# Optimization experiments

Hardware: AMD Instinct MI355X
Metric: run time of the kernel (lower is better)

The kernel has to match this reference:

```python
import jax, jax.numpy as jnp
import numpy as np

B, T, D, H, L, DFF, MAXLEN = 4, 2048, 512, 8, 6, 2048, 2048
DK = D // H
SCALE = float(1.0 / np.sqrt(DK * 2))  # 1/sqrt(d_k*2)


def layer_norm(x, g, b, eps=1e-5):
    m = jnp.mean(x, axis=-1, keepdims=True)
    v = jnp.var(x, axis=-1, keepdims=True)
    return (x - m) / jnp.sqrt(v + eps) * g + b


def setup_inputs() -> dict:
    key = jax.random.key(0)
    it = iter(jax.random.split(key, 48))
    def n(shape, std=0.02):
        return jax.random.normal(next(it), shape, dtype=jnp.float32) * std
    inp = {}
    inp['x'] = jax.random.normal(next(it), (B, T), dtype=jnp.float32)
    inp['ip_w'] = n((1, D)); inp['ip_b'] = jnp.zeros((D,))
    inp['ip_ln_g'] = jnp.ones((D,)); inp['ip_ln_b'] = jnp.zeros((D,))
    inp['pos_embed'] = n((MAXLEN, D), 0.01)
    inp['pad_token'] = n((D,), 0.01)
    inp['Wq'] = n((L, D, D)); inp['bq'] = jnp.zeros((L, D))
    inp['Wk'] = n((L, D, D)); inp['bk'] = jnp.zeros((L, D))
    inp['Wv'] = n((L, D, D)); inp['bv'] = jnp.zeros((L, D))
    inp['Wo'] = n((L, D, D)); inp['bo'] = jnp.zeros((L, D))
    inp['ln1_g'] = jnp.ones((L, D)); inp['ln1_b'] = jnp.zeros((L, D))
    inp['ln2_g'] = jnp.ones((L, D)); inp['ln2_b'] = jnp.zeros((L, D))
    inp['W1'] = n((L, D, DFF)); inp['b1'] = jnp.zeros((L, DFF))
    inp['W2'] = n((L, DFF, D)); inp['b2'] = jnp.zeros((L, D))
    inp['gate1'] = jnp.full((L,), 0.1); inp['gate2'] = jnp.full((L,), 0.1)
    inp['fn_g'] = jnp.ones((D,)); inp['fn_b'] = jnp.zeros((D,))
    for p in ['bh', 'ah', 'ch']:
        inp[p + '_ln_g'] = jnp.ones((D,)); inp[p + '_ln_b'] = jnp.zeros((D,))
    inp['bh_w'] = n((D, 2), 0.01); inp['bh_b'] = jnp.zeros((2,))
    inp['ah_w'] = n((D, 1), 0.01); inp['ah_b'] = jnp.zeros((1,))
    inp['ch_w'] = n((D, 1), 0.01); inp['ch_b'] = jnp.zeros((1,))
    return inp


def _forward(x, ip_w, ip_b, ip_ln_g, ip_ln_b, pos_embed, pad_token,
             Wq, bq, Wk, bk, Wv, bv, Wo, bo,
             ln1_g, ln1_b, ln2_g, ln2_b, W1, b1, W2, b2, gate1, gate2,
             fn_g, fn_b, bh_ln_g, bh_ln_b, bh_w, bh_b,
             ah_ln_g, ah_ln_b, ah_w, ah_b, ch_ln_g, ch_ln_b, ch_w, ch_b):
    Bx, Tx = x.shape
    xc = jnp.clip(x, -10.0, 10.0)
    pad_mask = xc == -1.0  # [B,T]
    h = layer_norm(xc[..., None] @ ip_w + ip_b, ip_ln_g, ip_ln_b)  # [B,T,D]
    h = h + 0.1 * pos_embed[None, :Tx, :]
    h = jnp.where(pad_mask[..., None], pad_token, h)
    cmask = jnp.triu(jnp.full((Tx, Tx), -10000.0, dtype=h.dtype), k=1)  # additive causal mask
    for i in range(L):
        xn = layer_norm(h, ln1_g[i], ln1_b[i])
        def heads(w, b, xn=xn):
            return (xn @ w + b).reshape(Bx, Tx, H, DK).transpose(0, 2, 1, 3)
        q = heads(Wq[i], bq[i]); k = heads(Wk[i], bk[i]); v = heads(Wv[i], bv[i])
        q = q / jnp.maximum(jnp.linalg.norm(q, axis=-1, keepdims=True), 1e-8)
        k = k / jnp.maximum(jnp.linalg.norm(k, axis=-1, keepdims=True), 1e-8)
        scores = jnp.clip(jnp.einsum('bhtd,bhsd->bhts', q, k) * SCALE, -5.0, 5.0) + cmask
        a = jax.nn.softmax(scores / 1.5, axis=-1)
        o = jnp.einsum('bhts,bhsd->bhtd', a, v).transpose(0, 2, 1, 3).reshape(Bx, Tx, D)
        h = h + gate1[i] * ((o @ Wo[i] + bo[i]) * 0.5)
        xn2 = layer_norm(h, ln2_g[i], ln2_b[i])
        ffn = jax.nn.gelu(xn2 @ W1[i] + b1[i], approximate=False) @ W2[i] + b2[i]
        h = jnp.clip(h + gate2[i] * ffn, -10.0, 10.0)
    h = layer_norm(h, fn_g, fn_b)
    m = (~pad_mask).astype(h.dtype)[..., None]
    mean = (h * m).sum(axis=1) / jnp.maximum(m.sum(axis=1), 1.0)  # masked mean pool [B,D]
    binary = layer_norm(mean, bh_ln_g, bh_ln_b) @ bh_w + bh_b
    anomaly = layer_norm(mean, ah_ln_g, ah_ln_b) @ ah_w + ah_b
    caustic = jax.nn.sigmoid(layer_norm(mean, ch_ln_g, ch_ln_b) @ ch_w + ch_b)
    return jnp.concatenate([binary, anomaly, caustic], axis=-1)  # [B,4]


def reference(x, ip_w, ip_b, ip_ln_g, ip_ln_b, pos_embed, pad_token,
              Wq, bq, Wk, bk, Wv, bv, Wo, bo,
              ln1_g, ln1_b, ln2_g, ln2_b, W1, b1, W2, b2, gate1, gate2,
              fn_g, fn_b, bh_ln_g, bh_ln_b, bh_w, bh_b,
              ah_ln_g, ah_ln_b, ah_w, ah_b, ch_ln_g, ch_ln_b, ch_w, ch_b):
    return _forward(x, ip_w, ip_b, ip_ln_g, ip_ln_b, pos_embed, pad_token,
                    Wq, bq, Wk, bk, Wv, bv, Wo, bo,
                    ln1_g, ln1_b, ln2_g, ln2_b, W1, b1, W2, b2, gate1, gate2,
                    fn_g, fn_b, bh_ln_g, bh_ln_b, bh_w, bh_b,
                    ah_ln_g, ah_ln_b, ah_w, ah_b, ch_ln_g, ch_ln_b, ch_w, ch_b)
```

## Files before the change

### kernel.cpp

```cpp
#include <hip/hip_runtime.h>
#include <hip/hip_bf16.h>
#include <math.h>

constexpr int Bsz = 4, T = 2048, D = 512, H = 8, Lnum = 6, DFF = 2048, DK = 64;
constexpr int QS2 = 1024;
constexpr float K2 = 0.08838834764831845f / 1.5f;

typedef __attribute__((ext_vector_type(8))) short svec8;
typedef __attribute__((ext_vector_type(4))) float fvec4;

__device__ __forceinline__ fvec4 mfma16(svec8 a, svec8 b, fvec4 c) {
    return __builtin_amdgcn_mfma_f32_16x16x32_bf16(a, b, c, 0, 0, 0);
}
__device__ __forceinline__ unsigned short f2b(float f) {
    unsigned int u = __float_as_uint(f);
    u += 0x7fffu + ((u >> 16) & 1u);
    return (unsigned short)(u >> 16);
}
__device__ __forceinline__ unsigned int pk2b(float a, float b) {
    __hip_bfloat162 h = __float22bfloat162_rn(float2{a, b});
    return *(unsigned int*)&h;
}
__device__ __forceinline__ float wave_red_sum(float v) {
    for (int o = 32; o > 0; o >>= 1) v += __shfl_down(v, o, 64);
    return __shfl(v, 0, 64);
}
__device__ __forceinline__ void glds16(const unsigned short* g, unsigned short* l) {
    __builtin_amdgcn_global_load_lds(
        (const __attribute__((address_space(1))) unsigned int*)g,
        (__attribute__((address_space(3))) unsigned int*)l, 16, 0, 0);
}
#define FRAG(buf, row, kq) (*(const svec8*)((buf) + (((row) << 6) | ((((kq) ^ ((row) & 7))) << 3))))

__global__ __launch_bounds__(64)
void embed_kernel(const float* __restrict__ x, const float* __restrict__ ip_w,
                  const float* __restrict__ ip_b, const float* __restrict__ g,
                  const float* __restrict__ bta, const float* __restrict__ pos,
                  const float* __restrict__ pad_tok, float* __restrict__ h)
{
    int row = blockIdx.x;
    int t = row & (T - 1);
    int lane = threadIdx.x;
    float xv = x[row];
    float xc = fminf(fmaxf(xv, -10.f), 10.f);
    bool pad = (xc == -1.0f);
    float pre[8];
    float s = 0.f, s2 = 0.f;
#pragma unroll
    for (int j = 0; j < 8; j++) {
        int d = j * 64 + lane;
        float p = xc * ip_w[d] + ip_b[d];
        pre[j] = p; s += p; s2 += p * p;
    }
    s = wave_red_sum(s); s2 = wave_red_sum(s2);
    float m = s * (1.f / 512.f);
    float var = s2 * (1.f / 512.f) - m * m;
    float rstd = 1.f / sqrtf(var + 1e-5f);
#pragma unroll
    for (int j = 0; j < 8; j++) {
        int d = j * 64 + lane;
        float hv = (pre[j] - m) * rstd * g[d] + bta[d] + 0.1f * pos[(size_t)t * D + d];
        if (pad) hv = pad_tok[d];
        h[(size_t)row * D + d] = hv;
    }
}

__global__ __launch_bounds__(256)
void ln_kernel(const float* __restrict__ in, float* __restrict__ out,
               const float* __restrict__ g, const float* __restrict__ b)
{
    int row = blockIdx.x * 4 + (threadIdx.x >> 6);
    int lane = threadIdx.x & 63;
    const float* r = in + (size_t)row * D;
    float4 v0 = ((const float4*)r)[lane];
    float4 v1 = ((const float4*)r)[lane + 64];
    float s = v0.x + v0.y + v0.z + v0.w + v1.x + v1.y + v1.z + v1.w;
    float s2 = v0.x*v0.x + v0.y*v0.y + v0.z*v0.z + v0.w*v0.w
             + v1.x*v1.x + v1.y*v1.y + v1.z*v1.z + v1.w*v1.w;
    s = wave_red_sum(s); s2 = wave_red_sum(s2);
    float m = s * (1.f / 512.f);
    float var = s2 * (1.f / 512.f) - m * m;
    float rstd = 1.f / sqrtf(var + 1e-5f);
    float4 g0 = ((const float4*)g)[lane], g1 = ((const float4*)g)[lane + 64];
    float4 b0 = ((const float4*)b)[lane], b1 = ((const float4*)b)[lane + 64];
    float4 o0, o1;
    o0.x = (v0.x - m) * rstd * g0.x + b0.x; o0.y = (v0.y - m) * rstd * g0.y + b0.y;
    o0.z = (v0.z - m) * rstd * g0.z + b0.z; o0.w = (v0.w - m) * rstd * g0.w + b0.w;
    o1.x = (v1.x - m) * rstd * g1.x + b1.x; o1.y = (v1.y - m) * rstd * g1.y + b1.y;
    o1.z = (v1.z - m) * rstd * g1.z + b1.z; o1.w = (v1.w - m) * rstd * g1.w + b1.w;
    ((float4*)(out + (size_t)row * D))[lane] = o0;
    ((float4*)(out + (size_t)row * D))[lane + 64] = o1;
}

__global__ __launch_bounds__(256)
void ln_bf16_kernel(const float* __restrict__ in, unsigned short* __restrict__ out,
                    const float* __restrict__ g, const float* __restrict__ b)
{
    int row = blockIdx.x * 4 + (threadIdx.x >> 6);
    int lane = threadIdx.x & 63;
    const float* r = in + (size_t)row * D;
    float4 v0 = ((const float4*)r)[lane];
    float4 v1 = ((const float4*)r)[lane + 64];
    float s = v0.x + v0.y + v0.z + v0.w + v1.x + v1.y + v1.z + v1.w;
    float s2 = v0.x*v0.x + v0.y*v0.y + v0.z*v0.z + v0.w*v0.w
             + v1.x*v1.x + v1.y*v1.y + v1.z*v1.z + v1.w*v1.w;
    s = wave_red_sum(s); s2 = wave_red_sum(s2);
    float m = s * (1.f / 512.f);
    float var = s2 * (1.f / 512.f) - m * m;
    float rstd = 1.f / sqrtf(var + 1e-5f);
    float4 g0 = ((const float4*)g)[lane], g1 = ((const float4*)g)[lane + 64];
    float4 b0 = ((const float4*)b)[lane], b1 = ((const float4*)b)[lane + 64];
    unsigned short o0[4], o1[4];
    o0[0] = f2b((v0.x - m) * rstd * g0.x + b0.x); o0[1] = f2b((v0.y - m) * rstd * g0.y + b0.y);
    o0[2] = f2b((v0.z - m) * rstd * g0.z + b0.z); o0[3] = f2b((v0.w - m) * rstd * g0.w + b0.w);
    o1[0] = f2b((v1.x - m) * rstd * g1.x + b1.x); o1[1] = f2b((v1.y - m) * rstd * g1.y + b1.y);
    o1[2] = f2b((v1.z - m) * rstd * g1.z + b1.z); o1[3] = f2b((v1.w - m) * rstd * g1.w + b1.w);
    *(uint2*)(out + (size_t)row * D + lane * 4) = *(uint2*)o0;
    *(uint2*)(out + (size_t)row * D + 256 + lane * 4) = *(uint2*)o1;
}

__global__ __launch_bounds__(256)
void wconv_kernel(const float* __restrict__ wq, const float* __restrict__ wk,
                  const float* __restrict__ wv, const float* __restrict__ wo,
                  const float* __restrict__ w1, const float* __restrict__ w2,
                  unsigned short* __restrict__ oq, unsigned short* __restrict__ ok,
                  unsigned short* __restrict__ ov, unsigned short* __restrict__ oo,
                  unsigned short* __restrict__ o1, unsigned short* __restrict__ o2)
{
    __shared__ float tile[32][33];
    int bid = blockIdx.x;
    const float* in; unsigned short* out; int K, N, kt, nt;
    if (bid < 1024) {
        int sel = bid >> 8, loc = bid & 255;
        in  = sel == 0 ? wq : sel == 1 ? wk : sel == 2 ? wv : wo;
        out = sel == 0 ? oq : sel == 1 ? ok : sel == 2 ? ov : oo;
        K = 512; N = 512; kt = loc >> 4; nt = loc & 15;
    } else if (bid < 2048) {
        int loc = bid - 1024; in = w1; out = o1; K = 512; N = 2048; kt = loc >> 6; nt = loc & 63;
    } else {
        int loc = bid - 2048; in = w2; out = o2; K = 2048; N = 512; kt = loc >> 4; nt = loc & 15;
    }
    int k0 = kt * 32, n0 = nt * 32;
    int t = threadIdx.x;
    int kr = t >> 3, nc = (t & 7) * 4;
    float4 v = *(const float4*)(in + (size_t)(k0 + kr) * N + n0 + nc);
    tile[kr][nc] = v.x; tile[kr][nc + 1] = v.y; tile[kr][nc + 2] = v.z; tile[kr][nc + 3] = v.w;
    __syncthreads();
    unsigned short o[4];
#pragma unroll
    for (int i = 0; i < 4; i++) o[i] = f2b(tile[nc + i][kr]);
    *(uint2*)(out + (size_t)(n0 + kr) * K + k0 + nc) = *(uint2*)o;
}

template<int EPI, int OBF, int BM>
__global__ __launch_bounds__(256)
void gemm_bf16(const unsigned short* __restrict__ A, const unsigned short* __restrict__ BT,
               const float* __restrict__ bias, const float* __restrict__ bias_b,
               const float* __restrict__ bias_c, const float* __restrict__ res,
               void* __restrict__ Cv, unsigned short* __restrict__ vtout,
               int M, int N, int K, const float* __restrict__ gate_p)
{
    constexpr int WN = (BM == 128) ? 2 : 4;
    constexpr int WSPAN = 128 / WN;
    constexpr int NT = WSPAN / 16;
    constexpr int MT = 4;
    constexpr int ACALLS = BM / 32;
    constexpr int SMEMSZ = (EPI == 0) ? 17408 : (BM * 64 + 128 * 64);
    __shared__ __align__(16) unsigned short SMEM[SMEMSZ];
    unsigned short* As = SMEM;
    unsigned short* Bs = SMEM + BM * 64;
    const int tid = threadIdx.x, w = tid >> 6, lane = tid & 63, quad = lane >> 4, ln = lane & 15;
    const int wm = w / WN, wn = w % WN;
    const int m0 = blockIdx.y * BM, n0 = blockIdx.x * 128;
    const int jg = (lane & 7) ^ ((lane >> 3) & 7);
    const int rb = w * 8 + (lane >> 3);
    const unsigned short* Agl = A + (size_t)(m0 + rb) * K + jg * 8;
    const unsigned short* Bgl = BT + (size_t)(n0 + rb) * K + jg * 8;

    fvec4 acc[MT][NT];
#pragma unroll
    for (int mt = 0; mt < MT; mt++)
#pragma unroll
        for (int nt = 0; nt < NT; nt++)
#pragma unroll
            for (int r = 0; r < 4; r++) acc[mt][nt][r] = 0.f;

    for (int k0 = 0; k0 < K; k0 += 64) {
        __syncthreads();
#pragma unroll
        for (int c = 0; c < ACALLS; c++)
            glds16(Agl + k0 + (size_t)c * 32 * K, As + c * 2048 + w * 512);
#pragma unroll
        for (int c = 0; c < 4; c++)
            glds16(Bgl + k0 + (size_t)c * 32 * K, Bs + c * 2048 + w * 512);
        __syncthreads();
#pragma unroll
        for (int kk = 0; kk < 2; kk++) {
            svec8 af[MT], bfr[NT];
#pragma unroll
            for (int mt = 0; mt < MT; mt++)
                af[mt] = FRAG(As, wm * 64 + mt * 16 + ln, kk * 4 + quad);
#pragma unroll
            for (int nt = 0; nt < NT; nt++)
                bfr[nt] = FRAG(Bs, wn * WSPAN + nt * 16 + ln, kk * 4 + quad);
#pragma unroll
            for (int mt = 0; mt < MT; mt++)
#pragma unroll
                for (int nt = 0; nt < NT; nt++)
                    acc[mt][nt] = mfma16(af[mt], bfr[nt], acc[mt][nt]);
        }
    }

    const float gate = (EPI == 1 || EPI == 3) ? gate_p[0] : 0.f;
    float bb[NT];
#pragma unroll
    for (int nt = 0; nt < NT; nt++) {
        int n = n0 + wn * WSPAN + nt * 16 + ln;
        if (EPI == 0) {
            int nseg = n >> 9;
            const float* bsel = nseg == 0 ? bias : (nseg == 1 ? bias_b : bias_c);
            bb[nt] = bsel[n - nseg * 512];
        } else {
            bb[nt] = bias[n];
        }
    }

    if (EPI == 0 && n0 >= 1024) {
        __syncthreads();
#pragma unroll
        for (int mt = 0; mt < MT; mt++) {
#pragma unroll
            for (int nt = 0; nt < NT; nt++) {
                int nl = wn * 64 + nt * 16 + ln;
                int mb = wm * 64 + mt * 16 + quad * 4;
                unsigned int lo = pk2b(acc[mt][nt][0] + bb[nt], acc[mt][nt][1] + bb[nt]);
                unsigned int hi = pk2b(acc[mt][nt][2] + bb[nt], acc[mt][nt][3] + bb[nt]);
                uint2 u; u.x = lo; u.y = hi;
                *(uint2*)(SMEM + nl * 136 + mb) = u;
            }
        }
        __syncthreads();
        int row = tid >> 1, half = (tid & 1) * 64;
        unsigned short* dst = vtout + ((size_t)((m0 >> 11) * 512 + (n0 - 1024) + row)) * T
                              + (m0 & (T - 1)) + half;
        const unsigned short* src = SMEM + row * 136 + half;
#pragma unroll
        for (int j = 0; j < 8; j++) *(uint4*)(dst + j * 8) = *(const uint4*)(src + j * 8);
        return;
    }

#pragma unroll
    for (int mt = 0; mt < MT; mt++) {
        float v[NT][4];
#pragma unroll
        for (int nt = 0; nt < NT; nt++)
#pragma unroll
            for (int r = 0; r < 4; r++) v[nt][r] = acc[mt][nt][r] + bb[nt];
        if (EPI == 0) {
#pragma unroll
            for (int r = 0; r < 4; r++) {
                float s = 0.f;
#pragma unroll
                for (int nt = 0; nt < NT; nt++) s += v[nt][r] * v[nt][r];
                s += __shfl_xor(s, 1); s += __shfl_xor(s, 2);
                s += __shfl_xor(s, 4); s += __shfl_xor(s, 8);
                float rs = 1.f / fmaxf(sqrtf(s), 1e-8f);
#pragma unroll
                for (int nt = 0; nt < NT; nt++) v[nt][r] *= rs;
            }
        }
#pragma unroll
        for (int nt = 0; nt < NT; nt++) {
            int n = n0 + wn * WSPAN + nt * 16 + ln;
#pragma unroll
            for (int r = 0; r < 4; r++) {
                int m = m0 + wm * 64 + mt * 16 + quad * 4 + r;
                float val = v[nt][r];
                if (EPI == 0) {
                    ((unsigned short*)Cv)[(size_t)m * QS2 + n] = f2b(val);
                } else {
                    size_t off = (size_t)m * N + n;
                    if (EPI == 1) val = res[off] + gate * 0.5f * val;
                    else if (EPI == 2) {
                        float u = val;
                        float z = 0.7978845608028654f * fmaf(0.044715f * u, u * u, u);
                        float e = __builtin_amdgcn_exp2f(z * 2.8853900817779268f);
                        float rr = __builtin_amdgcn_rcpf(e + 1.f);
                        val = u * (1.f - rr);
                    }
                    else if (EPI == 3) val = fminf(fmaxf(res[off] + gate * val, -10.f), 10.f);
                    if (OBF) ((unsigned short*)Cv)[off] = f2b(val);
                    else ((float*)Cv)[off] = val;
                }
            }
        }
    }
}

__device__ __forceinline__ void attn_step(
    const unsigned short* Q, unsigned short* Ps, const unsigned short* Ks, const unsigned short* Vt,
    bool diag, fvec4 (&oacc)[4], fvec4& lacc, int w, int quad, int ln)
{
    constexpr short BONE = (short)0x3F80;
    const svec8 ONES8 = {BONE, BONE, BONE, BONE, BONE, BONE, BONE, BONE};
    svec8 qf0 = FRAG(Q, w * 16 + ln, quad);
    svec8 qf1 = FRAG(Q, w * 16 + ln, 4 + quad);
    const int qrow = w * 16 + ln;
#pragma unroll
    for (int nt = 0; nt < 4; nt++) {
        fvec4 z; z[0] = z[1] = z[2] = z[3] = 0.f;
        z = mfma16(FRAG(Ks, nt * 16 + ln, quad), qf0, z);
        z = mfma16(FRAG(Ks, nt * 16 + ln, 4 + quad), qf1, z);
        const int sbase = nt * 16 + quad * 4;
        float p[4];
#pragma unroll
        for (int r = 0; r < 4; r++) {
            float y = z[r] * K2;
            float pv = fmaf(y, fmaf(y, 0.5f, 1.f), 1.f);
            if (diag && (sbase + r > qrow)) pv = 0.f;
            p[r] = pv;
        }
        uint2 u; u.x = pk2b(p[0], p[1]); u.y = pk2b(p[2], p[3]);
        int chunk = sbase >> 3, off = sbase & 7;
        *(uint2*)(Ps + ((qrow << 6) | ((chunk ^ (qrow & 7)) << 3) | off)) = u;
    }
#pragma unroll
    for (int ks = 0; ks < 2; ks++) {
        svec8 pa = FRAG(Ps, w * 16 + ln, ks * 4 + quad);
        lacc = mfma16(pa, ONES8, lacc);
#pragma unroll
        for (int nt = 0; nt < 4; nt++)
            oacc[nt] = mfma16(pa, FRAG(Vt, nt * 16 + ln, ks * 4 + quad), oacc[nt]);
    }
}

__global__ __launch_bounds__(256)
void attn_pair_kernel(const unsigned short* __restrict__ qkv, const unsigned short* __restrict__ vt,
                      unsigned short* __restrict__ o)
{
    __shared__ __align__(16) unsigned short QA[4096], QB[4096];
    __shared__ __align__(16) unsigned short K0[4096], V0[4096], K1[4096], V1[4096];
    __shared__ __align__(16) unsigned short Ps[4096];
    const int p = blockIdx.x, bh = blockIdx.y, b = bh >> 3, hh = bh & 7;
    const int qtA = p, qtB = 31 - p, nst = 32 - p;
    const int tid = threadIdx.x, w = tid >> 6, lane = tid & 63, quad = lane >> 4, ln = lane & 15;
    const int rl = lane >> 3, sl = lane & 7, jgz = sl ^ rl;
    const int w8 = w * 8;
    const int grow = w8 + rl;
    const unsigned short* qrow_p = qkv + ((size_t)(b * T) + grow) * QS2 + hh * 64 + jgz * 8;
    const unsigned short* krow_p = qrow_p + 512;
    const unsigned short* vrow_p = vt + ((size_t)(bh * 64) + grow) * T + jgz * 8;

    glds16(qrow_p + (size_t)(qtA * 64) * QS2, QA + w8 * 64);
    glds16(qrow_p + (size_t)(qtA * 64 + 32) * QS2, QA + (w8 + 32) * 64);
    glds16(qrow_p + (size_t)(qtB * 64) * QS2, QB + w8 * 64);
    glds16(qrow_p + (size_t)(qtB * 64 + 32) * QS2, QB + (w8 + 32) * 64);

    fvec4 oA[4], oB[4], lAv, lBv;
#pragma unroll
    for (int r = 0; r < 4; r++) { lAv[r] = 0.f; lBv[r] = 0.f; }
#pragma unroll
    for (int nt = 0; nt < 4; nt++)
#pragma unroll
        for (int r = 0; r < 4; r++) { oA[nt][r] = 0.f; oB[nt][r] = 0.f; }

    const int Nph = (nst + 1) >> 1;
    for (int ph = 0; ph < Nph; ph++) {
        const int s0 = 2 * ph, s1 = 2 * ph + 1;
        __syncthreads();
        glds16(krow_p + (size_t)(s0 * 64) * QS2, K0 + w8 * 64);
        glds16(krow_p + (size_t)(s0 * 64 + 32) * QS2, K0 + (w8 + 32) * 64);
        glds16(vrow_p + s0 * 64, V0 + w8 * 64);
        glds16(vrow_p + (size_t)32 * T + s0 * 64, V0 + (w8 + 32) * 64);
        if (s1 < nst) {
            glds16(krow_p + (size_t)(s1 * 64) * QS2, K1 + w8 * 64);
            glds16(krow_p + (size_t)(s1 * 64 + 32) * QS2, K1 + (w8 + 32) * 64);
            glds16(vrow_p + s1 * 64, V1 + w8 * 64);
            glds16(vrow_p + (size_t)32 * T + s1 * 64, V1 + (w8 + 32) * 64);
        }
        __syncthreads();
        attn_step(QB, Ps, K0, V0, s0 == nst - 1, oB, lBv, w, quad, ln);
        if (s0 <= p) attn_step(QA, Ps, K0, V0, s0 == p, oA, lAv, w, quad, ln);
        if (s1 < nst) {
            attn_step(QB, Ps, K1, V1, s1 == nst - 1, oB, lBv, w, quad, ln);
            if (s1 <= p) attn_step(QA, Ps, K1, V1, s1 == p, oA, lAv, w, quad, ln);
        }
    }

    unsigned short* ogA = o + (size_t)(b * T + qtA * 64 + w * 16 + quad * 4) * D + hh * 64;
    unsigned short* ogB = o + (size_t)(b * T + qtB * 64 + w * 16 + quad * 4) * D + hh * 64;
#pragma unroll
    for (int r = 0; r < 4; r++) {
        float ia = 1.f / lAv[r], ib = 1.f / lBv[r];
#pragma unroll
        for (int nt = 0; nt < 4; nt++) {
            ogA[(size_t)r * D + nt * 16 + ln] = f2b(oA[nt][r] * ia);
            ogB[(size_t)r * D + nt * 16 + ln] = f2b(oB[nt][r] * ib);
        }
    }
}

__global__ __launch_bounds__(256)
void pool_kernel(const float* __restrict__ hn, const float* __restrict__ x, float* __restrict__ part)
{
    int b = blockIdx.x, ch = blockIdx.y, tid = threadIdx.x;
    int t0 = ch * 128;
    float s0 = 0.f, s1 = 0.f, cnt = 0.f;
    for (int tt = 0; tt < 128; tt++) {
        int t = t0 + tt;
        float xv = x[b * T + t];
        float m = (xv == -1.0f) ? 0.f : 1.f;
        cnt += m;
        const float* r = hn + ((size_t)(b * T + t)) * D;
        s0 += r[tid] * m;
        s1 += r[tid + 256] * m;
    }
    float* pr = part + (size_t)(b * 16 + ch) * 513;
    pr[tid] = s0; pr[tid + 256] = s1;
    if (tid == 0) pr[512] = cnt;
}

__global__ __launch_bounds__(64)
void head_kernel(const float* __restrict__ part,
                 const float* __restrict__ bh_g, const float* __restrict__ bh_bl,
                 const float* __restrict__ ah_g, const float* __restrict__ ah_bl,
                 const float* __restrict__ ch_g, const float* __restrict__ ch_bl,
                 const float* __restrict__ bh_w, const float* __restrict__ bh_b2,
                 const float* __restrict__ ah_w, const float* __restrict__ ah_b2,
                 const float* __restrict__ ch_w, const float* __restrict__ ch_b2,
                 float* __restrict__ out)
{
    int b = blockIdx.x, lane = threadIdx.x;
    float cnt = 0.f;
    for (int c = 0; c < 16; c++) cnt += part[(size_t)(b * 16 + c) * 513 + 512];
    float denom = fmaxf(cnt, 1.f);
    float md[8];
    float s = 0.f, s2 = 0.f;
#pragma unroll
    for (int j = 0; j < 8; j++) {
        int d = j * 64 + lane;
        float acc = 0.f;
        for (int c = 0; c < 16; c++) acc += part[(size_t)(b * 16 + c) * 513 + d];
        md[j] = acc / denom;
        s += md[j]; s2 += md[j] * md[j];
    }
    s = wave_red_sum(s); s2 = wave_red_sum(s2);
    float mu = s * (1.f / 512.f);
    float var = s2 * (1.f / 512.f) - mu * mu;
    float rstd = 1.f / sqrtf(var + 1e-5f);
    float a0 = 0.f, a1 = 0.f, a2 = 0.f, a3 = 0.f;
#pragma unroll
    for (int j = 0; j < 8; j++) {
        int d = j * 64 + lane;
        float z = (md[j] - mu) * rstd;
        float zb = z * bh_g[d] + bh_bl[d];
        a0 += zb * bh_w[d * 2 + 0];
        a1 += zb * bh_w[d * 2 + 1];
        a2 += (z * ah_g[d] + ah_bl[d]) * ah_w[d];
        a3 += (z * ch_g[d] + ch_bl[d]) * ch_w[d];
    }
    a0 = wave_red_sum(a0); a1 = wave_red_sum(a1);
    a2 = wave_red_sum(a2); a3 = wave_red_sum(a3);
    if (lane == 0) {
        out[b * 4 + 0] = a0 + bh_b2[0];
        out[b * 4 + 1] = a1 + bh_b2[1];
        out[b * 4 + 2] = a2 + ah_b2[0];
        float t3 = a3 + ch_b2[0];
        out[b * 4 + 3] = 1.f / (1.f + expf(-t3));
    }
}

extern "C" void kernel_launch(void* const* d_in, const int* in_sizes, int n_in,
                              void* d_out, int out_size, void* d_ws, size_t ws_size,
                              hipStream_t stream)
{
    const float* x      = (const float*)d_in[0];
    const float* ip_w   = (const float*)d_in[1];
    const float* ip_b   = (const float*)d_in[2];
    const float* ip_ln_g= (const float*)d_in[3];
    const float* ip_ln_b= (const float*)d_in[4];
    const float* pos    = (const float*)d_in[5];
    const float* pad_tok= (const float*)d_in[6];
    const float* Wq = (const float*)d_in[7];  const float* bq = (const float*)d_in[8];
    const float* Wk = (const float*)d_in[9];  const float* bk = (const float*)d_in[10];
    const float* Wv = (const float*)d_in[11]; const float* bv = (const float*)d_in[12];
    const float* Wo = (const float*)d_in[13]; const float* bo = (const float*)d_in[14];
    const float* ln1_g = (const float*)d_in[15]; const float* ln1_b = (const float*)d_in[16];
    const float* ln2_g = (const float*)d_in[17]; const float* ln2_b = (const float*)d_in[18];
    const float* W1 = (const float*)d_in[19]; const float* b1 = (const float*)d_in[20];
    const float* W2 = (const float*)d_in[21]; const float* b2 = (const float*)d_in[22];
    const float* gate1 = (const float*)d_in[23]; const float* gate2 = (const float*)d_in[24];
    const float* fn_g = (const float*)d_in[25]; const float* fn_b = (const float*)d_in[26];
    const float* bh_g  = (const float*)d_in[27]; const float* bh_bl = (const float*)d_in[28];
    const float* ah_g  = (const float*)d_in[29]; const float* ah_bl = (const float*)d_in[30];
    const float* ch_g  = (const float*)d_in[31]; const float* ch_bl = (const float*)d_in[32];
    const float* bh_w  = (const float*)d_in[33]; const float* bh_b2 = (const float*)d_in[34];
    const float* ah_w  = (const float*)d_in[35]; const float* ah_b2 = (const float*)d_in[36];
    const float* ch_w  = (const float*)d_in[37]; const float* ch_b2 = (const float*)d_in[38];

    char* ws = (char*)d_ws;
    float*          h     = (float*)ws;
    unsigned short* act_b = (unsigned short*)(ws + 16777216);
    unsigned short* qkv   = (unsigned short*)(ws + 25165824);
    unsigned short* mid_b = (unsigned short*)(ws + 41943040);
    float*          xn_f  = (float*)(ws + 41943040);
    unsigned short* wT    = (unsigned short*)(ws + 75497472);
    unsigned short* vt    = (unsigned short*)(ws + 81788928);
    float*          part  = (float*)(ws + 90177536);
    float*          out   = (float*)d_out;

    unsigned short* wqT = wT;
    unsigned short* wkT = wT + 262144;
    unsigned short* wvT = wT + 524288;
    unsigned short* woT = wT + 786432;
    unsigned short* w1T = wT + 1048576;
    unsigned short* w2T = wT + 2097152;

    embed_kernel<<<dim3(Bsz * T), dim3(64), 0, stream>>>(x, ip_w, ip_b, ip_ln_g, ip_ln_b, pos, pad_tok, h);

    for (int i = 0; i < Lnum; i++) {
        const size_t dd = (size_t)i * D * D;
        const size_t df = (size_t)i * D * DFF;
        wconv_kernel<<<dim3(3072), dim3(256), 0, stream>>>(Wq + dd, Wk + dd, Wv + dd, Wo + dd,
                                                           W1 + df, W2 + df,
                                                           wqT, wkT, wvT, woT, w1T, w2T);
        ln_bf16_kernel<<<dim3(Bsz * T / 4), dim3(256), 0, stream>>>(h, act_b, ln1_g + i * D, ln1_b + i * D);
        gemm_bf16<0, 1, 128><<<dim3(12, 64), dim3(256), 0, stream>>>(act_b, wqT, bq + i * D, bk + i * D, bv + i * D,
                                                                     nullptr, qkv, vt, Bsz * T, 1536, D, nullptr);
        attn_pair_kernel<<<dim3(16, 32), dim3(256), 0, stream>>>(qkv, vt, act_b);
        gemm_bf16<1, 0, 64><<<dim3(4, 128), dim3(256), 0, stream>>>(act_b, woT, bo + i * D, nullptr, nullptr,
                                                                    h, h, nullptr, Bsz * T, D, D, gate1 + i);
        ln_bf16_kernel<<<dim3(Bsz * T / 4), dim3(256), 0, stream>>>(h, act_b, ln2_g + i * D, ln2_b + i * D);
        gemm_bf16<2, 1, 128><<<dim3(16, 64), dim3(256), 0, stream>>>(act_b, w1T, b1 + i * DFF, nullptr, nullptr,
                                                                     nullptr, mid_b, nullptr, Bsz * T, DFF, D, nullptr);
        gemm_bf16<3, 0, 64><<<dim3(4, 128), dim3(256), 0, stream>>>(mid_b, w2T, b2 + i * D, nullptr, nullptr,
                                                                    h, h, nullptr, Bsz * T, D, DFF, gate2 + i);
    }

    ln_kernel<<<dim3(Bsz * T / 4), dim3(256), 0, stream>>>(h, xn_f, fn_g, fn_b);
    pool_kernel<<<dim3(Bsz, 16), dim3(256), 0, stream>>>(xn_f, x, part);
    head_kernel<<<dim3(Bsz), dim3(64), 0, stream>>>(part, bh_g, bh_bl, ah_g, ah_bl, ch_g, ch_bl,
                                                    bh_w, bh_b2, ah_w, ah_b2, ch_w, ch_b2, out);
}
```

Measured before the change: 1.228 ms.

## Swap GEMM grid axes, XCD-aware attention block mapping, fold scale into Q

GEMM launches now put M tiles on blockIdx.x and N tiles on blockIdx.y, so neighbouring blocks share weight columns and A-row reuse in L2 changes. The attention grid is flattened and remapped so each XCD handles a fixed set of batch-heads, aiming to keep K/V for a head in one XCD's L2. The K2 scale is folded into the Q normalisation in the QKV epilogue, which removes a multiply per score. The attention step is templated on the diagonal flag so the mask check is compiled out for off-diagonal tiles.

```diff
diff --git a/kernel.cpp b/kernel.cpp
--- a/kernel.cpp
+++ b/kernel.cpp
@@ -171,7 +171,7 @@
     unsigned short* Bs = SMEM + BM * 64;
     const int tid = threadIdx.x, w = tid >> 6, lane = tid & 63, quad = lane >> 4, ln = lane & 15;
     const int wm = w / WN, wn = w % WN;
-    const int m0 = blockIdx.y * BM, n0 = blockIdx.x * 128;
+    const int m0 = blockIdx.x * BM, n0 = blockIdx.y * 128;
     const int jg = (lane & 7) ^ ((lane >> 3) & 7);
     const int rb = w * 8 + (lane >> 3);
     const unsigned short* Agl = A + (size_t)(m0 + rb) * K + jg * 8;
@@ -257,6 +257,7 @@
 #pragma unroll
             for (int r = 0; r < 4; r++) v[nt][r] = acc[mt][nt][r] + bb[nt];
         if (EPI == 0) {
+            const float fac = ((n0 + wn * WSPAN) < 512) ? K2 : 1.f;
 #pragma unroll
             for (int r = 0; r < 4; r++) {
                 float s = 0.f;
@@ -264,7 +265,7 @@
                 for (int nt = 0; nt < NT; nt++) s += v[nt][r] * v[nt][r];
                 s += __shfl_xor(s, 1); s += __shfl_xor(s, 2);
                 s += __shfl_xor(s, 4); s += __shfl_xor(s, 8);
-                float rs = 1.f / fmaxf(sqrtf(s), 1e-8f);
+                float rs = fac / fmaxf(sqrtf(s), 1e-8f);
 #pragma unroll
                 for (int nt = 0; nt < NT; nt++) v[nt][r] *= rs;
             }
@@ -297,9 +298,10 @@
     }
 }
 
+template<bool DIAG>
 __device__ __forceinline__ void attn_step(
     const unsigned short* Q, unsigned short* Ps, const unsigned short* Ks, const unsigned short* Vt,
-    bool diag, fvec4 (&oacc)[4], fvec4& lacc, int w, int quad, int ln)
+    fvec4 (&oacc)[4], fvec4& lacc, int w, int quad, int ln)
 {
     constexpr short BONE = (short)0x3F80;
     const svec8 ONES8 = {BONE, BONE, BONE, BONE, BONE, BONE, BONE, BONE};
@@ -315,9 +317,9 @@
         float p[4];
 #pragma unroll
         for (int r = 0; r < 4; r++) {
-            float y = z[r] * K2;
+            float y = z[r];
             float pv = fmaf(y, fmaf(y, 0.5f, 1.f), 1.f);
-            if (diag && (sbase + r > qrow)) pv = 0.f;
+            if (DIAG && (sbase + r > qrow)) pv = 0.f;
             p[r] = pv;
         }
         uint2 u; u.x = pk2b(p[0], p[1]); u.y = pk2b(p[2], p[3]);
@@ -341,7 +343,11 @@
     __shared__ __align__(16) unsigned short QA[4096], QB[4096];
     __shared__ __align__(16) unsigned short K0[4096], V0[4096], K1[4096], V1[4096];
     __shared__ __align__(16) unsigned short Ps[4096];
-    const int p = blockIdx.x, bh = blockIdx.y, b = bh >> 3, hh = bh & 7;
+    const int fid = blockIdx.x;
+    const int xcd = fid & 7, slot = fid >> 3;
+    const int bh = xcd * 4 + (slot & 3);
+    const int p = slot >> 2;
+    const int b = bh >> 3, hh = bh & 7;
     const int qtA = p, qtB = 31 - p, nst = 32 - p;
     const int tid = threadIdx.x, w = tid >> 6, lane = tid & 63, quad = lane >> 4, ln = lane & 15;
     const int rl = lane >> 3, sl = lane & 7, jgz = sl ^ rl;
@@ -379,11 +385,19 @@
             glds16(vrow_p + (size_t)32 * T + s1 * 64, V1 + (w8 + 32) * 64);
         }
         __syncthreads();
-        attn_step(QB, Ps, K0, V0, s0 == nst - 1, oB, lBv, w, quad, ln);
-        if (s0 <= p) attn_step(QA, Ps, K0, V0, s0 == p, oA, lAv, w, quad, ln);
+        if (s0 == nst - 1) attn_step<true >(QB, Ps, K0, V0, oB, lBv, w, quad, ln);
+        else               attn_step<false>(QB, Ps, K0, V0, oB, lBv, w, quad, ln);
+        if (s0 <= p) {
+            if (s0 == p) attn_step<true >(QA, Ps, K0, V0, oA, lAv, w, quad, ln);
+            else         attn_step<false>(QA, Ps, K0, V0, oA, lAv, w, quad, ln);
+        }
         if (s1 < nst) {
-            attn_step(QB, Ps, K1, V1, s1 == nst - 1, oB, lBv, w, quad, ln);
-            if (s1 <= p) attn_step(QA, Ps, K1, V1, s1 == p, oA, lAv, w, quad, ln);
+            if (s1 == nst - 1) attn_step<true >(QB, Ps, K1, V1, oB, lBv, w, quad, ln);
+            else               attn_step<false>(QB, Ps, K1, V1, oB, lBv, w, quad, ln);
+            if (s1 <= p) {
+                if (s1 == p) attn_step<true >(QA, Ps, K1, V1, oA, lAv, w, quad, ln);
+                else         attn_step<false>(QA, Ps, K1, V1, oA, lAv, w, quad, ln);
+            }
         }
     }
 
@@ -525,15 +539,15 @@
                                                            W1 + df, W2 + df,
                                                            wqT, wkT, wvT, woT, w1T, w2T);
         ln_bf16_kernel<<<dim3(Bsz * T / 4), dim3(256), 0, stream>>>(h, act_b, ln1_g + i * D, ln1_b + i * D);
-        gemm_bf16<0, 1, 128><<<dim3(12, 64), dim3(256), 0, stream>>>(act_b, wqT, bq + i * D, bk + i * D, bv + i * D,
+        gemm_bf16<0, 1, 128><<<dim3(64, 12), dim3(256), 0, stream>>>(act_b, wqT, bq + i * D, bk + i * D, bv + i * D,
                                                                      nullptr, qkv, vt, Bsz * T, 1536, D, nullptr);
-        attn_pair_kernel<<<dim3(16, 32), dim3(256), 0, stream>>>(qkv, vt, act_b);
-        gemm_bf16<1, 0, 64><<<dim3(4, 128), dim3(256), 0, stream>>>(act_b, woT, bo + i * D, nullptr, nullptr,
+        attn_pair_kernel<<<dim3(512), dim3(256), 0, stream>>>(qkv, vt, act_b);
+        gemm_bf16<1, 0, 64><<<dim3(128, 4), dim3(256), 0, stream>>>(act_b, woT, bo + i * D, nullptr, nullptr,
                                                                     h, h, nullptr, Bsz * T, D, D, gate1 + i);
         ln_bf16_kernel<<<dim3(Bsz * T / 4), dim3(256), 0, stream>>>(h, act_b, ln2_g + i * D, ln2_b + i * D);
-        gemm_bf16<2, 1, 128><<<dim3(16, 64), dim3(256), 0, stream>>>(act_b, w1T, b1 + i * DFF, nullptr, nullptr,
+        gemm_bf16<2, 1, 128><<<dim3(64, 16), dim3(256), 0, stream>>>(act_b, w1T, b1 + i * DFF, nullptr, nullptr,
                                                                      nullptr, mid_b, nullptr, Bsz * T, DFF, D, nullptr);
-        gemm_bf16<3, 0, 64><<<dim3(4, 128), dim3(256), 0, stream>>>(mid_b, w2T, b2 + i * D, nullptr, nullptr,
+        gemm_bf16<3, 0, 64><<<dim3(128, 4), dim3(256), 0, stream>>>(mid_b, w2T, b2 + i * D, nullptr, nullptr,
                                                                     h, h, nullptr, Bsz * T, D, DFF, gate2 + i);
     }
 
```

After: 1.134 ms. 1.08x faster.
